# Optimization experiments

Hardware: AMD Instinct MI355X
Metric: run time of the kernel (lower is better)

Reference implementation:

```python
import jax, jax.numpy as jnp
import numpy as np

INF = 1e10
D_KEY = 64

def setup_inputs() -> dict:
    key = jax.random.key(0)
    k1, k2, k3 = jax.random.split(key, 3)
    B, S, D = 4, 4096, D_KEY
    return {
        "query": jax.random.normal(k1, (B, S, D), dtype=jnp.float32),
        "key": jax.random.normal(k2, (B, S, D), dtype=jnp.float32),
        "value": jax.random.normal(k3, (B, S, D), dtype=jnp.float32),
        "mask": jnp.ones((B, S), dtype=jnp.float32),
    }

def reference(query, key, value, mask):
    # dot_products: [B, Sq, Sk]
    dot = jnp.einsum('bqd,bkd->bqk', query, key)
    S = key.shape[1]
    # causal: subtract INF on strict upper triangle (triu(1))
    tri = jnp.triu(jnp.ones((S, S), dtype=dot.dtype), 1) * INF
    dot = dot - tri[None, :, :]
    # additive padding mask: subtract (1-mask)*INF broadcast over query dim
    dot = dot - (1.0 - mask)[:, None, :] * INF
    scale = jnp.sqrt(jnp.float32(D_KEY))
    probs = jax.nn.softmax(dot / scale, axis=-1)  # [B, Sq, Sk]
    # dropout ratio = 0.0 -> identity
    return jnp.einsum('bqk,bkd->bqd', probs, value)
```

## Files before the change

### kernel.cpp

```cpp
#include <hip/hip_runtime.h>
#include <hip/hip_bf16.h>


#define S_LEN  4096
#define N_B    4
#define NT64   64
#define BIGF   1.803368e9f
#define QSCALE (0.125f * 1.44269504089f)
#define FIXMAX 11.0f
#define BIGNEG 1.25e9f
#define MADD_PAD 4224

typedef __attribute__((ext_vector_type(8))) short short8;
typedef __attribute__((ext_vector_type(4))) float f32x4;
typedef __attribute__((ext_vector_type(2))) unsigned int uint2v;
typedef unsigned short ushort_t;

#define KT2_OFF   0
#define KT2_BYTES (N_B * NT64 * 4096 * 2)
#define VT2_OFF   (KT2_OFF + KT2_BYTES)
#define VT2_BYTES (N_B * NT64 * 4096 * 2)
#define NSLOT     (N_B * 184 * 4)
#define OP_OFF    (VT2_OFF + VT2_BYTES)
#define OP_BYTES  (NSLOT * 1024 * 4)
#define PLS_OFF   (OP_OFF + OP_BYTES)
#define PLS_BYTES (NSLOT * 32 * 4)
#define MADD_OFF  (PLS_OFF + PLS_BYTES)
#define MADD_BYTES (N_B * MADD_PAD * 4)
#define WS10_NEEDED (MADD_OFF + MADD_BYTES)

__device__ __forceinline__ unsigned short f2bf(float f) {
    union { float f; unsigned u; } v; v.f = f;
    unsigned r = v.u + 0x7FFF + ((v.u >> 16) & 1);
    return (unsigned short)(r >> 16);
}
__device__ __forceinline__ float bflo(unsigned u) {
    union { unsigned u; float f; } v; v.u = u << 16; return v.f;
}
__device__ __forceinline__ float bfhi(unsigned u) {
    union { unsigned u; float f; } v; v.u = u & 0xffff0000u; return v.f;
}
__device__ __forceinline__ void ld_lds16(const void* g, void* l) {
    __builtin_amdgcn_global_load_lds((const __attribute__((address_space(1))) void*)g,
                                     (__attribute__((address_space(3))) void*)l, 16, 0, 0);
}
__device__ __forceinline__ void ld_lds4(const void* g, void* l) {
    __builtin_amdgcn_global_load_lds((const __attribute__((address_space(1))) void*)g,
                                     (__attribute__((address_space(3))) void*)l, 4, 0, 0);
}


__global__ __launch_bounds__(256)
void prep6(const float* __restrict__ K, const float* __restrict__ V,
           const float* __restrict__ M,
           ushort_t* __restrict__ Kt, ushort_t* __restrict__ Vt,
           float* __restrict__ Madd)
{
    const int t = blockIdx.x, b = blockIdx.y, tid = threadIdx.x;
    ushort_t* ko = Kt + ((size_t)(b * NT64 + t)) * 4096;
    ushort_t* vo = Vt + ((size_t)(b * NT64 + t)) * 4096;
    #pragma unroll
    for (int i = 0; i < 2; ++i) {
        const int idx = tid + 256 * i;
        const int row = idx >> 3, cc = idx & 7;
        const float* src = K + ((size_t)(b * S_LEN + t * 64 + row)) * 64 + cc * 8;
        const f32x4 a = *(const f32x4*)src;
        const f32x4 d4 = *(const f32x4*)(src + 4);
        short8 w;
        w[0]=(short)f2bf(a[0]); w[1]=(short)f2bf(a[1]); w[2]=(short)f2bf(a[2]); w[3]=(short)f2bf(a[3]);
        w[4]=(short)f2bf(d4[0]); w[5]=(short)f2bf(d4[1]); w[6]=(short)f2bf(d4[2]); w[7]=(short)f2bf(d4[3]);
        *(short8*)(ko + row * 64 + ((cc ^ (row & 7)) << 3)) = w;
    }
    #pragma unroll
    for (int i = 0; i < 2; ++i) {
        const int idx = tid + 256 * i;
        const int cc = idx >> 6, d = idx & 63;
        short8 w;
        #pragma unroll
        for (int j = 0; j < 8; ++j)
            w[j] = (short)f2bf(V[((size_t)(b * S_LEN + t * 64 + cc * 8 + j)) * 64 + d]);
        *(short8*)(vo + d * 64 + ((cc ^ (d & 7)) << 3)) = w;
    }
    if (tid < 64) {
        const int k = t * 64 + tid;
        Madd[b * MADD_PAD + k] = (1.0f - M[b * S_LEN + k]) * BIGF;
    }
}

#define PTRANS(PA, PB, PF) do {                                                     \
    unsigned c00_, c01_, c10_, c11_;                                                \
    __asm__("v_cvt_pk_bf16_f32 %0, %1, %2" : "=v"(c00_) : "v"(PA[0]), "v"(PA[1])); \
    __asm__("v_cvt_pk_bf16_f32 %0, %1, %2" : "=v"(c01_) : "v"(PA[2]), "v"(PA[3])); \
    __asm__("v_cvt_pk_bf16_f32 %0, %1, %2" : "=v"(c10_) : "v"(PB[0]), "v"(PB[1])); \
    __asm__("v_cvt_pk_bf16_f32 %0, %1, %2" : "=v"(c11_) : "v"(PB[2]), "v"(PB[3])); \
    uint2v s0_ = __builtin_amdgcn_permlane32_swap(c00_, c10_, false, false);        \
    uint2v s1_ = __builtin_amdgcn_permlane32_swap(c01_, c11_, false, false);        \
    unsigned a0_ = s0_.x, b0_ = s0_.y, a1_ = s1_.x, b1_ = s1_.y;                    \
    __asm__("v_permlane16_swap_b32 %0, %1" : "+v"(a0_), "+v"(b0_));                 \
    __asm__("v_permlane16_swap_b32 %0, %1" : "+v"(a1_), "+v"(b1_));                 \
    union { unsigned u[4]; short8 s; } pw_;                                         \
    pw_.u[0] = a0_;                                                                 \
    pw_.u[1] = a1_;                                                                 \
    pw_.u[2] = b0_;                                                                 \
    pw_.u[3] = b1_;                                                                 \
    PF = pw_.s;                                                                     \
} while (0)

#define CMASK(SV, BB, QG) do {                     \
    _Pragma("unroll")                              \
    for (int r_ = 0; r_ < 4; ++r_)                 \
        if ((BB) + r_ > (QG)) SV[r_] -= BIGF;      \
} while (0)

__global__ __launch_bounds__(256, 3)
void attn_fa13(const float* __restrict__ Q, const ushort_t* __restrict__ Kt,
               const ushort_t* __restrict__ Vt, const float* __restrict__ Madd,
               unsigned* __restrict__ Opu, float* __restrict__ Pll,
               float* __restrict__ O)
{
    const int x = 186 - blockIdx.x;
    const int b = blockIdx.y;
    int v = 1;
    #pragma unroll
    for (int vv = 2; vv <= 11; ++vv) v += (x >= (3 * vv * (vv - 1)) / 2) ? 1 : 0;
    const int y  = x - (3 * v * (v - 1)) / 2;
    const int T  = 3 * (v - 1) + y / v;
    const int c  = y - (y / v) * v;
    const int nt = 2 * T + 2;
    const int t0 = 6 * c;
    const int t1 = (t0 + 6 < nt) ? t0 + 6 : nt;

    const int wid  = threadIdx.x >> 6;
    const int lane = threadIdx.x & 63, l15 = lane & 15, g = lane >> 4;
    const int qbase = T * 128 + wid * 32;
    const int dtile = 2 * T + (wid >> 1);
    const int qg0 = 32 * (wid & 1) + l15 - 4 * g;
    const int qg1 = qg0 + 16;

    __shared__ __attribute__((aligned(16))) ushort_t Kb[3][4096];
    __shared__ __attribute__((aligned(16))) ushort_t Vb[3][4096];
    __shared__ __attribute__((aligned(16))) float    Ml[3][4][64];

    const float* Q0 = Q + ((size_t)(b * S_LEN + qbase + l15)) * 64 + g * 8;
    short8 qA0, qA1, qB0, qB1;
    {
        const f32x4 a0 = *(const f32x4*)(Q0);
        const f32x4 a1 = *(const f32x4*)(Q0 + 4);
        const f32x4 a2 = *(const f32x4*)(Q0 + 32);
        const f32x4 a3 = *(const f32x4*)(Q0 + 36);
        const float* Q1 = Q0 + 16 * 64;
        const f32x4 b0 = *(const f32x4*)(Q1);
        const f32x4 b1 = *(const f32x4*)(Q1 + 4);
        const f32x4 b2 = *(const f32x4*)(Q1 + 32);
        const f32x4 b3 = *(const f32x4*)(Q1 + 36);
        #pragma unroll
        for (int j = 0; j < 4; ++j) {
            qA0[j]     = (short)f2bf(a0[j] * QSCALE);
            qA0[4 + j] = (short)f2bf(a1[j] * QSCALE);
            qA1[j]     = (short)f2bf(a2[j] * QSCALE);
            qA1[4 + j] = (short)f2bf(a3[j] * QSCALE);
            qB0[j]     = (short)f2bf(b0[j] * QSCALE);
            qB0[4 + j] = (short)f2bf(b1[j] * QSCALE);
            qB1[j]     = (short)f2bf(b2[j] * QSCALE);
            qB1[4 + j] = (short)f2bf(b3[j] * QSCALE);
        }
    }
    short8 ones8;
    #pragma unroll
    for (int j = 0; j < 8; ++j) ones8[j] = (short)0x3F80;

    const char*  KtB  = (const char*)Kt + (size_t)b * (NT64 * 8192);
    const char*  VtB  = (const char*)Vt + (size_t)b * (NT64 * 8192);
    const float* MaBs = Madd + (size_t)b * MADD_PAD;

    f32x4 accA[5], accB[5];
    #pragma unroll
    for (int dt = 0; dt < 5; ++dt) {
        accA[dt] = (f32x4){0.f, 0.f, 0.f, 0.f};
        accB[dt] = (f32x4){0.f, 0.f, 0.f, 0.f};
    }

    auto stage = [&](int sl, int t_) {
        const char* kg = KtB + (size_t)t_ * 8192 + wid * 2048 + lane * 16;
        char* kl = (char*)&Kb[sl][0] + wid * 2048;
        ld_lds16(kg,        kl);
        ld_lds16(kg + 1024, kl + 1024);
        const char* vg = VtB + (size_t)t_ * 8192 + wid * 2048 + lane * 16;
        char* vl = (char*)&Vb[sl][0] + wid * 2048;
        ld_lds16(vg,        vl);
        ld_lds16(vg + 1024, vl + 1024);
        ld_lds4 (MaBs + (size_t)t_ * 64 + lane, &Ml[sl][wid][0]);
    };

    stage(0, t0);
    if (t0 + 1 < t1) stage(1, t0 + 1);

    const int ch0 = ((g ^ (l15 & 7)) << 3);
    const int ch1 = (((4 | g) ^ (l15 & 7)) << 3);

    int sc = 0;
    for (int t = t0; t < t1; ++t) {
        if (t + 1 < t1) {
            __asm__ volatile("s_waitcnt vmcnt(5)" ::: "memory");
        } else {
            __asm__ volatile("s_waitcnt vmcnt(0)" ::: "memory");
        }
        __builtin_amdgcn_s_barrier();
        __builtin_amdgcn_sched_barrier(0);

        const int sn = (sc + 2 > 2) ? sc - 1 : sc + 2;
        if (t + 2 < t1) stage(sn, t + 2);

        if (t <= dtile) {
            const ushort_t* kbase = &Kb[sc][0];
            const ushort_t* vbase = &Vb[sc][0];
            const float*    mlw   = &Ml[sc][wid][0];
            const f32x4 z_ = (f32x4){0.f, 0.f, 0.f, 0.f};

            #pragma unroll
            for (int h = 0; h < 2; ++h) {
                const int rb = 32 * h;
                const int chh = h ? ch1 : ch0;
                const f32x4 mmE = *(const f32x4*)(mlw + rb + 4 * g);
                const f32x4 mmO = *(const f32x4*)(mlw + rb + 16 + 4 * g);

                short8 ke0 = *(const short8*)(kbase + ((rb + l15) << 6) + ch0);
                short8 ke1 = *(const short8*)(kbase + ((rb + l15) << 6) + ch1);
                short8 ko0 = *(const short8*)(kbase + ((rb + 16 + l15) << 6) + ch0);
                short8 ko1 = *(const short8*)(kbase + ((rb + 16 + l15) << 6) + ch1);

                f32x4 sEA = __builtin_amdgcn_mfma_f32_16x16x32_bf16(ke0, qA0, z_, 0, 0, 0);
                f32x4 sOA = __builtin_amdgcn_mfma_f32_16x16x32_bf16(ko0, qA0, z_, 0, 0, 0);
                f32x4 sEB = __builtin_amdgcn_mfma_f32_16x16x32_bf16(ke0, qB0, z_, 0, 0, 0);
                f32x4 sOB = __builtin_amdgcn_mfma_f32_16x16x32_bf16(ko0, qB0, z_, 0, 0, 0);
                sEA = __builtin_amdgcn_mfma_f32_16x16x32_bf16(ke1, qA1, sEA, 0, 0, 0);
                sOA = __builtin_amdgcn_mfma_f32_16x16x32_bf16(ko1, qA1, sOA, 0, 0, 0);
                sEB = __builtin_amdgcn_mfma_f32_16x16x32_bf16(ke1, qB1, sEB, 0, 0, 0);
                sOB = __builtin_amdgcn_mfma_f32_16x16x32_bf16(ko1, qB1, sOB, 0, 0, 0);

                sEA -= mmE; sOA -= mmO; sEB -= mmE; sOB -= mmO;
                if (t == dtile) {
                    CMASK(sEA, rb, qg0);      CMASK(sOA, rb + 16, qg0);
                    CMASK(sEB, rb, qg1);      CMASK(sOB, rb + 16, qg1);
                }

                float pEA[4], pOA[4], pEB[4], pOB[4];
                #pragma unroll
                for (int r = 0; r < 4; ++r) {
                    pEA[r] = exp2f(sEA[r] - FIXMAX);
                    pOA[r] = exp2f(sOA[r] - FIXMAX);
                    pEB[r] = exp2f(sEB[r] - FIXMAX);
                    pOB[r] = exp2f(sOB[r] - FIXMAX);
                }

                short8 pfA, pfB;
                PTRANS(pEA, pOA, pfA);
                PTRANS(pEB, pOB, pfB);

                short8 v0 = *(const short8*)(vbase + ((0  + l15) << 6) + chh);
                short8 v1 = *(const short8*)(vbase + ((16 + l15) << 6) + chh);
                short8 v2 = *(const short8*)(vbase + ((32 + l15) << 6) + chh);
                short8 v3 = *(const short8*)(vbase + ((48 + l15) << 6) + chh);
                __builtin_amdgcn_s_setprio(1);
                accA[0] = __builtin_amdgcn_mfma_f32_16x16x32_bf16(pfA, v0, accA[0], 0, 0, 0);
                accA[1] = __builtin_amdgcn_mfma_f32_16x16x32_bf16(pfA, v1, accA[1], 0, 0, 0);
                accA[2] = __builtin_amdgcn_mfma_f32_16x16x32_bf16(pfA, v2, accA[2], 0, 0, 0);
                accA[3] = __builtin_amdgcn_mfma_f32_16x16x32_bf16(pfA, v3, accA[3], 0, 0, 0);
                accA[4] = __builtin_amdgcn_mfma_f32_16x16x32_bf16(pfA, ones8, accA[4], 0, 0, 0);
                accB[0] = __builtin_amdgcn_mfma_f32_16x16x32_bf16(pfB, v0, accB[0], 0, 0, 0);
                accB[1] = __builtin_amdgcn_mfma_f32_16x16x32_bf16(pfB, v1, accB[1], 0, 0, 0);
                accB[2] = __builtin_amdgcn_mfma_f32_16x16x32_bf16(pfB, v2, accB[2], 0, 0, 0);
                accB[3] = __builtin_amdgcn_mfma_f32_16x16x32_bf16(pfB, v3, accB[3], 0, 0, 0);
                accB[4] = __builtin_amdgcn_mfma_f32_16x16x32_bf16(pfB, ones8, accB[4], 0, 0, 0);
                __builtin_amdgcn_s_setprio(0);
            }
        }
        sc = (sc == 2) ? 0 : sc + 1;
    }

    if (v == 1) {
        float* Ob = O + ((size_t)(b * S_LEN + qbase)) * 64;
        #pragma unroll
        for (int r = 0; r < 4; ++r) {
            const float ila = 1.0f / accA[4][r];
            const float ilb = 1.0f / accB[4][r];
            #pragma unroll
            for (int dt = 0; dt < 4; ++dt) {
                Ob[(4 * g + r) * 64 + 16 * dt + l15]      = accA[dt][r] * ila;
                Ob[(16 + 4 * g + r) * 64 + 16 * dt + l15] = accB[dt][r] * ilb;
            }
        }
    } else {
        const int slot = (b * 184 + (x - 3)) * 4 + wid;
        unsigned* Os = Opu + (size_t)slot * 1024;
        #pragma unroll
        for (int dt = 0; dt < 4; ++dt) {
            unsigned u0, u1, u2, u3;
            __asm__("v_cvt_pk_bf16_f32 %0, %1, %2" : "=v"(u0) : "v"(accA[dt][0]), "v"(accA[dt][1]));
            __asm__("v_cvt_pk_bf16_f32 %0, %1, %2" : "=v"(u1) : "v"(accA[dt][2]), "v"(accA[dt][3]));
            __asm__("v_cvt_pk_bf16_f32 %0, %1, %2" : "=v"(u2) : "v"(accB[dt][0]), "v"(accB[dt][1]));
            __asm__("v_cvt_pk_bf16_f32 %0, %1, %2" : "=v"(u3) : "v"(accB[dt][2]), "v"(accB[dt][3]));
            const int d = 16 * dt + l15;
            Os[(2 * g + 0) * 64 + d]     = u0;
            Os[(2 * g + 1) * 64 + d]     = u1;
            Os[(8 + 2 * g + 0) * 64 + d] = u2;
            Os[(8 + 2 * g + 1) * 64 + d] = u3;
        }
        if (l15 == 0) {
            #pragma unroll
            for (int r = 0; r < 4; ++r) {
                Pll[slot * 32 + 4 * g + r]      = accA[4][r];
                Pll[slot * 32 + 16 + 4 * g + r] = accB[4][r];
            }
        }
    }
}

__global__ __launch_bounds__(256)
void combine6(const unsigned* __restrict__ Opu, const float* __restrict__ Pll,
              float* __restrict__ O)
{
    const int bx = blockIdx.x, b = blockIdx.y;
    const int T = 3 + (bx >> 2), wv = bx & 3;
    const int v = (T + 3) / 3;
    const int x0 = (3 * v * (v - 1)) / 2 + (T - 3 * (v - 1)) * v;
    const int sb = (b * 184 + (x0 - 3)) * 4 + wv;
    const int tid = threadIdx.x, rg = tid >> 6, d = tid & 63;

    float a[8] = {0.f,0.f,0.f,0.f,0.f,0.f,0.f,0.f};
    float l[8] = {0.f,0.f,0.f,0.f,0.f,0.f,0.f,0.f};
    for (int cc = 0; cc < v; ++cc) {
        const int sl = sb + 4 * cc;
        const unsigned* base = &Opu[(size_t)sl * 1024 + d];
        const unsigned w0 = base[(4 * rg + 0) * 64];
        const unsigned w1 = base[(4 * rg + 1) * 64];
        const unsigned w2 = base[(4 * rg + 2) * 64];
        const unsigned w3 = base[(4 * rg + 3) * 64];
        a[0] += bflo(w0); a[1] += bfhi(w0);
        a[2] += bflo(w1); a[3] += bfhi(w1);
        a[4] += bflo(w2); a[5] += bfhi(w2);
        a[6] += bflo(w3); a[7] += bfhi(w3);
        #pragma unroll
        for (int j = 0; j < 8; ++j)
            l[j] += Pll[sl * 32 + 8 * rg + j];
    }
    float* Ob = O + ((size_t)(b * S_LEN + T * 128 + wv * 32 + 8 * rg)) * 64 + d;
    #pragma unroll
    for (int j = 0; j < 8; ++j)
        Ob[(size_t)j * 64] = a[j] / l[j];
}


__global__ __launch_bounds__(256)
void attn_fwd_fb(const float* __restrict__ Q, const float* __restrict__ K,
                 const float* __restrict__ V, const float* __restrict__ M,
                 float* __restrict__ O)
{
    const int tile  = blockIdx.x;
    const int b     = blockIdx.y;
    const int qbase = tile * 64;
    const int tid   = threadIdx.x;
    const int wave  = tid >> 6;
    const int lane  = tid & 63;
    const int l15   = lane & 15;
    const int g     = lane >> 4;

    __shared__ __attribute__((aligned(16))) unsigned short Klds[32 * 64];
    __shared__ __attribute__((aligned(16))) unsigned short Vtlds[64 * 40];
    __shared__ __attribute__((aligned(16))) unsigned short Plds[4][16 * 40];

    const float* Qb = Q + ((size_t)b * S_LEN + qbase) * 64;
    const float* Kb = K + (size_t)b * S_LEN * 64;
    const float* Vb = V + (size_t)b * S_LEN * 64;
    const float* Mb = M + (size_t)b * S_LEN;

    const int qrow = 16 * wave + l15;
    short8 qf[2];
    #pragma unroll
    for (int dc = 0; dc < 2; ++dc) {
        const float* src = Qb + (size_t)qrow * 64 + dc * 32 + g * 8;
        #pragma unroll
        for (int j = 0; j < 8; ++j) qf[dc][j] = (short)f2bf(src[j] * 0.125f);
    }

    f32x4 acc[4];
    #pragma unroll
    for (int dt = 0; dt < 4; ++dt) acc[dt] = (f32x4){0.f, 0.f, 0.f, 0.f};
    float mrow[4], lrow[4];
    #pragma unroll
    for (int r = 0; r < 4; ++r) { mrow[r] = -1e30f; lrow[r] = 0.f; }

    const int q_max_wave = qbase + 16 * wave + 15;
    const int nkv = (qbase + 64) / 32;

    for (int it = 0; it < nkv; ++it) {
        const int kv = it * 32;
        __syncthreads();
        {
            const int k = tid >> 3, c = tid & 7;
            const float* src = Kb + (size_t)(kv + k) * 64 + c * 8;
            short8 t8;
            #pragma unroll
            for (int j = 0; j < 8; ++j) t8[j] = (short)f2bf(src[j]);
            const int byte = k * 128 + ((c * 16) ^ ((k & 7) << 4));
            *(short8*)((char*)Klds + byte) = t8;
        }
        {
            const int k = tid & 31, dch = tid >> 5;
            const float* src = Vb + (size_t)(kv + k) * 64 + dch * 8;
            #pragma unroll
            for (int j = 0; j < 8; ++j)
                Vtlds[(dch * 8 + j) * 40 + k] = f2bf(src[j]);
        }
        __syncthreads();

        if (kv > q_max_wave) continue;

        f32x4 s[2];
        s[0] = (f32x4){0.f,0.f,0.f,0.f};
        s[1] = (f32x4){0.f,0.f,0.f,0.f};
        #pragma unroll
        for (int kt = 0; kt < 2; ++kt) {
            const int krow = 16 * kt + l15;
            #pragma unroll
            for (int dc = 0; dc < 2; ++dc) {
                const int byte = krow * 128 + ((dc * 64 + g * 16) ^ ((krow & 7) << 4));
                short8 kf = *(const short8*)((const char*)Klds + byte);
                s[kt] = __builtin_amdgcn_mfma_f32_16x16x32_bf16(qf[dc], kf, s[kt], 0, 0, 0);
            }
        }

        float mk0 = Mb[kv + l15];
        float mk1 = Mb[kv + 16 + l15];
        #pragma unroll
        for (int kt = 0; kt < 2; ++kt) {
            const int gk = kv + 16 * kt + l15;
            const float madd = (1.0f - (kt ? mk1 : mk0)) * BIGNEG;
            #pragma unroll
            for (int r = 0; r < 4; ++r) {
                const int gq = qbase + 16 * wave + 4 * g + r;
                float vv = s[kt][r] - madd;
                if (gk > gq) vv -= BIGNEG;
                s[kt][r] = vv;
            }
        }

        float pexp[2][4], alpha[4];
        #pragma unroll
        for (int r = 0; r < 4; ++r) {
            float tm = fmaxf(s[0][r], s[1][r]);
            #pragma unroll
            for (int off = 8; off >= 1; off >>= 1)
                tm = fmaxf(tm, __shfl_xor(tm, off, 64));
            const float mnew = fmaxf(mrow[r], tm);
            const float a  = __expf(mrow[r] - mnew);
            const float p0 = __expf(s[0][r] - mnew);
            const float p1 = __expf(s[1][r] - mnew);
            float rs = p0 + p1;
            #pragma unroll
            for (int off = 8; off >= 1; off >>= 1)
                rs += __shfl_xor(rs, off, 64);
            lrow[r] = lrow[r] * a + rs;
            mrow[r] = mnew;
            alpha[r] = a;
            pexp[0][r] = p0; pexp[1][r] = p1;
        }

        #pragma unroll
        for (int dt = 0; dt < 4; ++dt)
            #pragma unroll
            for (int r = 0; r < 4; ++r)
                acc[dt][r] *= alpha[r];

        unsigned short* P = Plds[wave];
        #pragma unroll
        for (int kt = 0; kt < 2; ++kt)
            #pragma unroll
            for (int r = 0; r < 4; ++r)
                P[(4 * g + r) * 40 + 16 * kt + l15] = f2bf(pexp[kt][r]);

        __asm__ volatile("s_waitcnt lgkmcnt(0)" ::: "memory");

        short8 pf = *(const short8*)((const char*)P + (l15 * 40 + g * 8) * 2);
        #pragma unroll
        for (int dt = 0; dt < 4; ++dt) {
            short8 vf = *(const short8*)((const char*)Vtlds + ((dt * 16 + l15) * 40 + g * 8) * 2);
            acc[dt] = __builtin_amdgcn_mfma_f32_16x16x32_bf16(pf, vf, acc[dt], 0, 0, 0);
        }
    }

    float* Ob = O + ((size_t)b * S_LEN + qbase) * 64;
    #pragma unroll
    for (int r = 0; r < 4; ++r) {
        const float inv = 1.0f / lrow[r];
        const int row = 16 * wave + 4 * g + r;
        #pragma unroll
        for (int dt = 0; dt < 4; ++dt)
            Ob[(size_t)row * 64 + dt * 16 + l15] = acc[dt][r] * inv;
    }
}

extern "C" void kernel_launch(void* const* d_in, const int* in_sizes, int n_in,
                              void* d_out, int out_size, void* d_ws, size_t ws_size,
                              hipStream_t stream) {
    const float* Q = (const float*)d_in[0];
    const float* K = (const float*)d_in[1];
    const float* V = (const float*)d_in[2];
    const float* M = (const float*)d_in[3];
    float* O = (float*)d_out;

    if (ws_size >= (size_t)WS10_NEEDED) {
        ushort_t* Kt = (ushort_t*)((char*)d_ws + KT2_OFF);
        ushort_t* Vt = (ushort_t*)((char*)d_ws + VT2_OFF);
        unsigned* Op = (unsigned*)((char*)d_ws + OP_OFF);
        float*    Pll= (float*)((char*)d_ws + PLS_OFF);
        float*    Ma = (float*)((char*)d_ws + MADD_OFF);
        prep6<<<dim3(NT64, N_B), 256, 0, stream>>>(K, V, M, Kt, Vt, Ma);
        attn_fa13<<<dim3(187, N_B), 256, 0, stream>>>(Q, Kt, Vt, Ma, Op, Pll, O);
        combine6<<<dim3(116, N_B), 256, 0, stream>>>(Op, Pll, O);
    } else {
        dim3 grid(S_LEN / 64, N_B);
        attn_fwd_fb<<<grid, 256, 0, stream>>>(Q, K, V, M, O);
    }
}
```

Baseline: 40.49 us.

## Fuse prep, attention and combine into one cooperative kernel with grid syncs

Merges the three kernels (K/V bf16 conversion, split attention, partial-result combine) into a single cooperative launch that separates the phases with grid-wide barriers. This removes two kernel launch gaps and the tail/ramp between dependent kernels. The launch first checks occupancy (748 blocks need at least 3 per CU across 256 CUs) and falls back to the three-kernel path otherwise. The cost is two grid.sync barriers, the cooperative launch overhead, and all blocks waiting on the slowest attention block before combine starts.

```diff
diff --git a/kernel.cpp b/kernel.cpp
--- a/kernel.cpp
+++ b/kernel.cpp
@@ -1,5 +1,8 @@
 #include <hip/hip_runtime.h>
 #include <hip/hip_bf16.h>
+#include <hip/hip_cooperative_groups.h>
+
+namespace cg = cooperative_groups;
 
 
 #define S_LEN  4096
@@ -10,6 +13,8 @@
 #define FIXMAX 11.0f
 #define BIGNEG 1.25e9f
 #define MADD_PAD 4224
+#define NJOB   187
+#define NGRID  (NJOB * N_B)
 
 typedef __attribute__((ext_vector_type(8))) short short8;
 typedef __attribute__((ext_vector_type(4))) float f32x4;
@@ -47,44 +52,6 @@
 __device__ __forceinline__ void ld_lds4(const void* g, void* l) {
     __builtin_amdgcn_global_load_lds((const __attribute__((address_space(1))) void*)g,
                                      (__attribute__((address_space(3))) void*)l, 4, 0, 0);
-}
-
-
-__global__ __launch_bounds__(256)
-void prep6(const float* __restrict__ K, const float* __restrict__ V,
-           const float* __restrict__ M,
-           ushort_t* __restrict__ Kt, ushort_t* __restrict__ Vt,
-           float* __restrict__ Madd)
-{
-    const int t = blockIdx.x, b = blockIdx.y, tid = threadIdx.x;
-    ushort_t* ko = Kt + ((size_t)(b * NT64 + t)) * 4096;
-    ushort_t* vo = Vt + ((size_t)(b * NT64 + t)) * 4096;
-    #pragma unroll
-    for (int i = 0; i < 2; ++i) {
-        const int idx = tid + 256 * i;
-        const int row = idx >> 3, cc = idx & 7;
-        const float* src = K + ((size_t)(b * S_LEN + t * 64 + row)) * 64 + cc * 8;
-        const f32x4 a = *(const f32x4*)src;
-        const f32x4 d4 = *(const f32x4*)(src + 4);
-        short8 w;
-        w[0]=(short)f2bf(a[0]); w[1]=(short)f2bf(a[1]); w[2]=(short)f2bf(a[2]); w[3]=(short)f2bf(a[3]);
-        w[4]=(short)f2bf(d4[0]); w[5]=(short)f2bf(d4[1]); w[6]=(short)f2bf(d4[2]); w[7]=(short)f2bf(d4[3]);
-        *(short8*)(ko + row * 64 + ((cc ^ (row & 7)) << 3)) = w;
-    }
-    #pragma unroll
-    for (int i = 0; i < 2; ++i) {
-        const int idx = tid + 256 * i;
-        const int cc = idx >> 6, d = idx & 63;
-        short8 w;
-        #pragma unroll
-        for (int j = 0; j < 8; ++j)
-            w[j] = (short)f2bf(V[((size_t)(b * S_LEN + t * 64 + cc * 8 + j)) * 64 + d]);
-        *(short8*)(vo + d * 64 + ((cc ^ (d & 7)) << 3)) = w;
-    }
-    if (tid < 64) {
-        const int k = t * 64 + tid;
-        Madd[b * MADD_PAD + k] = (1.0f - M[b * S_LEN + k]) * BIGF;
-    }
 }
 
 #define PTRANS(PA, PB, PF) do {                                                     \
@@ -112,14 +79,49 @@
         if ((BB) + r_ > (QG)) SV[r_] -= BIGF;      \
 } while (0)
 
-__global__ __launch_bounds__(256, 3)
-void attn_fa13(const float* __restrict__ Q, const ushort_t* __restrict__ Kt,
-               const ushort_t* __restrict__ Vt, const float* __restrict__ Madd,
-               unsigned* __restrict__ Opu, float* __restrict__ Pll,
-               float* __restrict__ O)
-{
-    const int x = 186 - blockIdx.x;
-    const int b = blockIdx.y;
+
+__device__ __forceinline__ void prep_body(int t, int b, int tid,
+    const float* __restrict__ K, const float* __restrict__ V,
+    const float* __restrict__ M,
+    ushort_t* __restrict__ Kt, ushort_t* __restrict__ Vt,
+    float* __restrict__ Madd)
+{
+    ushort_t* ko = Kt + ((size_t)(b * NT64 + t)) * 4096;
+    ushort_t* vo = Vt + ((size_t)(b * NT64 + t)) * 4096;
+    #pragma unroll
+    for (int i = 0; i < 2; ++i) {
+        const int idx = tid + 256 * i;
+        const int row = idx >> 3, cc = idx & 7;
+        const float* src = K + ((size_t)(b * S_LEN + t * 64 + row)) * 64 + cc * 8;
+        const f32x4 a = *(const f32x4*)src;
+        const f32x4 d4 = *(const f32x4*)(src + 4);
+        short8 w;
+        w[0]=(short)f2bf(a[0]); w[1]=(short)f2bf(a[1]); w[2]=(short)f2bf(a[2]); w[3]=(short)f2bf(a[3]);
+        w[4]=(short)f2bf(d4[0]); w[5]=(short)f2bf(d4[1]); w[6]=(short)f2bf(d4[2]); w[7]=(short)f2bf(d4[3]);
+        *(short8*)(ko + row * 64 + ((cc ^ (row & 7)) << 3)) = w;
+    }
+    #pragma unroll
+    for (int i = 0; i < 2; ++i) {
+        const int idx = tid + 256 * i;
+        const int cc = idx >> 6, d = idx & 63;
+        short8 w;
+        #pragma unroll
+        for (int j = 0; j < 8; ++j)
+            w[j] = (short)f2bf(V[((size_t)(b * S_LEN + t * 64 + cc * 8 + j)) * 64 + d]);
+        *(short8*)(vo + d * 64 + ((cc ^ (d & 7)) << 3)) = w;
+    }
+    if (tid < 64) {
+        const int k = t * 64 + tid;
+        Madd[b * MADD_PAD + k] = (1.0f - M[b * S_LEN + k]) * BIGF;
+    }
+}
+
+__device__ __forceinline__ void attn_body(int x, int b, int tid,
+    ushort_t* Kb , ushort_t* Vb , float* Ml ,
+    const float* __restrict__ Q, const ushort_t* __restrict__ Kt,
+    const ushort_t* __restrict__ Vt, const float* __restrict__ Madd,
+    unsigned* __restrict__ Opu, float* __restrict__ Pll, float* __restrict__ O)
+{
     int v = 1;
     #pragma unroll
     for (int vv = 2; vv <= 11; ++vv) v += (x >= (3 * vv * (vv - 1)) / 2) ? 1 : 0;
@@ -130,16 +132,12 @@
     const int t0 = 6 * c;
     const int t1 = (t0 + 6 < nt) ? t0 + 6 : nt;
 
-    const int wid  = threadIdx.x >> 6;
-    const int lane = threadIdx.x & 63, l15 = lane & 15, g = lane >> 4;
+    const int wid  = tid >> 6;
+    const int lane = tid & 63, l15 = lane & 15, g = lane >> 4;
     const int qbase = T * 128 + wid * 32;
     const int dtile = 2 * T + (wid >> 1);
     const int qg0 = 32 * (wid & 1) + l15 - 4 * g;
     const int qg1 = qg0 + 16;
-
-    __shared__ __attribute__((aligned(16))) ushort_t Kb[3][4096];
-    __shared__ __attribute__((aligned(16))) ushort_t Vb[3][4096];
-    __shared__ __attribute__((aligned(16))) float    Ml[3][4][64];
 
     const float* Q0 = Q + ((size_t)(b * S_LEN + qbase + l15)) * 64 + g * 8;
     short8 qA0, qA1, qB0, qB1;
@@ -182,14 +180,14 @@
 
     auto stage = [&](int sl, int t_) {
         const char* kg = KtB + (size_t)t_ * 8192 + wid * 2048 + lane * 16;
-        char* kl = (char*)&Kb[sl][0] + wid * 2048;
+        char* kl = (char*)(Kb + sl * 4096) + wid * 2048;
         ld_lds16(kg,        kl);
         ld_lds16(kg + 1024, kl + 1024);
         const char* vg = VtB + (size_t)t_ * 8192 + wid * 2048 + lane * 16;
-        char* vl = (char*)&Vb[sl][0] + wid * 2048;
+        char* vl = (char*)(Vb + sl * 4096) + wid * 2048;
         ld_lds16(vg,        vl);
         ld_lds16(vg + 1024, vl + 1024);
-        ld_lds4 (MaBs + (size_t)t_ * 64 + lane, &Ml[sl][wid][0]);
+        ld_lds4 (MaBs + (size_t)t_ * 64 + lane, Ml + (sl * 4 + wid) * 64);
     };
 
     stage(0, t0);
@@ -212,9 +210,9 @@
         if (t + 2 < t1) stage(sn, t + 2);
 
         if (t <= dtile) {
-            const ushort_t* kbase = &Kb[sc][0];
-            const ushort_t* vbase = &Vb[sc][0];
-            const float*    mlw   = &Ml[sc][wid][0];
+            const ushort_t* kbase = Kb + sc * 4096;
+            const ushort_t* vbase = Vb + sc * 4096;
+            const float*    mlw   = Ml + (sc * 4 + wid) * 64;
             const f32x4 z_ = (f32x4){0.f, 0.f, 0.f, 0.f};
 
             #pragma unroll
@@ -316,16 +314,15 @@
     }
 }
 
-__global__ __launch_bounds__(256)
-void combine6(const unsigned* __restrict__ Opu, const float* __restrict__ Pll,
-              float* __restrict__ O)
-{
-    const int bx = blockIdx.x, b = blockIdx.y;
+__device__ __forceinline__ void combine_body(int bx, int b, int tid,
+    const unsigned* __restrict__ Opu, const float* __restrict__ Pll,
+    float* __restrict__ O)
+{
     const int T = 3 + (bx >> 2), wv = bx & 3;
     const int v = (T + 3) / 3;
     const int x0 = (3 * v * (v - 1)) / 2 + (T - 3 * (v - 1)) * v;
     const int sb = (b * 184 + (x0 - 3)) * 4 + wv;
-    const int tid = threadIdx.x, rg = tid >> 6, d = tid & 63;
+    const int rg = tid >> 6, d = tid & 63;
 
     float a[8] = {0.f,0.f,0.f,0.f,0.f,0.f,0.f,0.f};
     float l[8] = {0.f,0.f,0.f,0.f,0.f,0.f,0.f,0.f};
@@ -351,6 +348,70 @@
 }
 
 
+__global__ __launch_bounds__(256, 3)
+void attn_mono(const float* __restrict__ Q, const float* __restrict__ K,
+               const float* __restrict__ V, const float* __restrict__ M,
+               ushort_t* __restrict__ Kt, ushort_t* __restrict__ Vt,
+               float* __restrict__ Madd,
+               unsigned* __restrict__ Opu, float* __restrict__ Pll,
+               float* __restrict__ O)
+{
+    cg::grid_group grid = cg::this_grid();
+    const int gid = blockIdx.x;
+    const int tid = threadIdx.x;
+
+    __shared__ __attribute__((aligned(16))) ushort_t Kb[3 * 4096];
+    __shared__ __attribute__((aligned(16))) ushort_t Vb[3 * 4096];
+    __shared__ __attribute__((aligned(16))) float    Ml[3 * 4 * 64];
+
+    if (gid < 256)
+        prep_body(gid & 63, gid >> 6, tid, K, V, M, Kt, Vt, Madd);
+
+    grid.sync();
+
+    {
+        const int b = gid / NJOB;
+        const int x = 186 - (gid - b * NJOB);
+        attn_body(x, b, tid, Kb, Vb, Ml, Q, Kt, Vt, Madd, Opu, Pll, O);
+    }
+
+    grid.sync();
+
+    if (gid < 464)
+        combine_body(gid % 116, gid / 116, tid, Opu, Pll, O);
+}
+
+
+__global__ __launch_bounds__(256)
+void prep6(const float* __restrict__ K, const float* __restrict__ V,
+           const float* __restrict__ M,
+           ushort_t* __restrict__ Kt, ushort_t* __restrict__ Vt,
+           float* __restrict__ Madd)
+{
+    prep_body(blockIdx.x, blockIdx.y, threadIdx.x, K, V, M, Kt, Vt, Madd);
+}
+
+__global__ __launch_bounds__(256, 3)
+void attn_fa13(const float* __restrict__ Q, const ushort_t* __restrict__ Kt,
+               const ushort_t* __restrict__ Vt, const float* __restrict__ Madd,
+               unsigned* __restrict__ Opu, float* __restrict__ Pll,
+               float* __restrict__ O)
+{
+    __shared__ __attribute__((aligned(16))) ushort_t Kb[3 * 4096];
+    __shared__ __attribute__((aligned(16))) ushort_t Vb[3 * 4096];
+    __shared__ __attribute__((aligned(16))) float    Ml[3 * 4 * 64];
+    attn_body(186 - blockIdx.x, blockIdx.y, threadIdx.x, Kb, Vb, Ml,
+              Q, Kt, Vt, Madd, Opu, Pll, O);
+}
+
+__global__ __launch_bounds__(256)
+void combine6(const unsigned* __restrict__ Opu, const float* __restrict__ Pll,
+              float* __restrict__ O)
+{
+    combine_body(blockIdx.x, blockIdx.y, threadIdx.x, Opu, Pll, O);
+}
+
+
 __global__ __launch_bounds__(256)
 void attn_fwd_fb(const float* __restrict__ Q, const float* __restrict__ K,
                  const float* __restrict__ V, const float* __restrict__ M,
@@ -515,8 +576,21 @@
         unsigned* Op = (unsigned*)((char*)d_ws + OP_OFF);
         float*    Pll= (float*)((char*)d_ws + PLS_OFF);
         float*    Ma = (float*)((char*)d_ws + MADD_OFF);
+
+        int blocksPerCU = 0;
+        hipError_t qerr = hipOccupancyMaxActiveBlocksPerMultiprocessor(
+            &blocksPerCU, (const void*)attn_mono, 256, 0);
+        bool coop_ok = (qerr == hipSuccess) && (blocksPerCU * 256 >= NGRID);
+        if (coop_ok) {
+            void* args[] = { (void*)&Q, (void*)&K, (void*)&V, (void*)&M,
+                             (void*)&Kt, (void*)&Vt, (void*)&Ma,
+                             (void*)&Op, (void*)&Pll, (void*)&O };
+            hipError_t lerr = hipLaunchCooperativeKernel(
+                (const void*)attn_mono, dim3(NGRID), dim3(256), args, 0, stream);
+            if (lerr == hipSuccess) return;
+        }
         prep6<<<dim3(NT64, N_B), 256, 0, stream>>>(K, V, M, Kt, Vt, Ma);
-        attn_fa13<<<dim3(187, N_B), 256, 0, stream>>>(Q, Kt, Vt, Ma, Op, Pll, O);
+        attn_fa13<<<dim3(NJOB, N_B), 256, 0, stream>>>(Q, Kt, Vt, Ma, Op, Pll, O);
         combine6<<<dim3(116, N_B), 256, 0, stream>>>(Op, Pll, O);
     } else {
         dim3 grid(S_LEN / 64, N_B);
```

Measured after the change: 40.63 us. No clear change (+0.3%).

## Fuse split-KV combine into attention kernel via last-block atomic counter

Applied to the files above, without the earlier changes.

Removes the separate combine kernel launch. Each split-KV block publishes its partial output, then increments a per-query-tile atomic counter. The block that arrives last performs the reduction and writes the final output. Counters are zeroed in the prep kernel. This saves one launch and its tail, at the cost of threadfences, an atomic, and a serialized combine on the last-arriving block.

```diff
diff --git a/kernel.cpp b/kernel.cpp
--- a/kernel.cpp
+++ b/kernel.cpp
@@ -10,6 +10,7 @@
 #define FIXMAX 11.0f
 #define BIGNEG 1.25e9f
 #define MADD_PAD 4224
+#define NJOB   187
 
 typedef __attribute__((ext_vector_type(8))) short short8;
 typedef __attribute__((ext_vector_type(4))) float f32x4;
@@ -27,7 +28,9 @@
 #define PLS_BYTES (NSLOT * 32 * 4)
 #define MADD_OFF  (PLS_OFF + PLS_BYTES)
 #define MADD_BYTES (N_B * MADD_PAD * 4)
-#define WS10_NEEDED (MADD_OFF + MADD_BYTES)
+#define CNT_OFF   (MADD_OFF + MADD_BYTES)
+#define CNT_BYTES (N_B * 29 * 4)
+#define WS11_NEEDED (CNT_OFF + CNT_BYTES)
 
 __device__ __forceinline__ unsigned short f2bf(float f) {
     union { float f; unsigned u; } v; v.f = f;
@@ -47,44 +50,6 @@
 __device__ __forceinline__ void ld_lds4(const void* g, void* l) {
     __builtin_amdgcn_global_load_lds((const __attribute__((address_space(1))) void*)g,
                                      (__attribute__((address_space(3))) void*)l, 4, 0, 0);
-}
-
-
-__global__ __launch_bounds__(256)
-void prep6(const float* __restrict__ K, const float* __restrict__ V,
-           const float* __restrict__ M,
-           ushort_t* __restrict__ Kt, ushort_t* __restrict__ Vt,
-           float* __restrict__ Madd)
-{
-    const int t = blockIdx.x, b = blockIdx.y, tid = threadIdx.x;
-    ushort_t* ko = Kt + ((size_t)(b * NT64 + t)) * 4096;
-    ushort_t* vo = Vt + ((size_t)(b * NT64 + t)) * 4096;
-    #pragma unroll
-    for (int i = 0; i < 2; ++i) {
-        const int idx = tid + 256 * i;
-        const int row = idx >> 3, cc = idx & 7;
-        const float* src = K + ((size_t)(b * S_LEN + t * 64 + row)) * 64 + cc * 8;
-        const f32x4 a = *(const f32x4*)src;
-        const f32x4 d4 = *(const f32x4*)(src + 4);
-        short8 w;
-        w[0]=(short)f2bf(a[0]); w[1]=(short)f2bf(a[1]); w[2]=(short)f2bf(a[2]); w[3]=(short)f2bf(a[3]);
-        w[4]=(short)f2bf(d4[0]); w[5]=(short)f2bf(d4[1]); w[6]=(short)f2bf(d4[2]); w[7]=(short)f2bf(d4[3]);
-        *(short8*)(ko + row * 64 + ((cc ^ (row & 7)) << 3)) = w;
-    }
-    #pragma unroll
-    for (int i = 0; i < 2; ++i) {
-        const int idx = tid + 256 * i;
-        const int cc = idx >> 6, d = idx & 63;
-        short8 w;
-        #pragma unroll
-        for (int j = 0; j < 8; ++j)
-            w[j] = (short)f2bf(V[((size_t)(b * S_LEN + t * 64 + cc * 8 + j)) * 64 + d]);
-        *(short8*)(vo + d * 64 + ((cc ^ (d & 7)) << 3)) = w;
-    }
-    if (tid < 64) {
-        const int k = t * 64 + tid;
-        Madd[b * MADD_PAD + k] = (1.0f - M[b * S_LEN + k]) * BIGF;
-    }
 }
 
 #define PTRANS(PA, PB, PF) do {                                                     \
@@ -112,11 +77,83 @@
         if ((BB) + r_ > (QG)) SV[r_] -= BIGF;      \
 } while (0)
 
+
+__global__ __launch_bounds__(256)
+void prep6(const float* __restrict__ K, const float* __restrict__ V,
+           const float* __restrict__ M,
+           ushort_t* __restrict__ Kt, ushort_t* __restrict__ Vt,
+           float* __restrict__ Madd, unsigned* __restrict__ Cnt)
+{
+    const int t = blockIdx.x, b = blockIdx.y, tid = threadIdx.x;
+    ushort_t* ko = Kt + ((size_t)(b * NT64 + t)) * 4096;
+    ushort_t* vo = Vt + ((size_t)(b * NT64 + t)) * 4096;
+    #pragma unroll
+    for (int i = 0; i < 2; ++i) {
+        const int idx = tid + 256 * i;
+        const int row = idx >> 3, cc = idx & 7;
+        const float* src = K + ((size_t)(b * S_LEN + t * 64 + row)) * 64 + cc * 8;
+        const f32x4 a = *(const f32x4*)src;
+        const f32x4 d4 = *(const f32x4*)(src + 4);
+        short8 w;
+        w[0]=(short)f2bf(a[0]); w[1]=(short)f2bf(a[1]); w[2]=(short)f2bf(a[2]); w[3]=(short)f2bf(a[3]);
+        w[4]=(short)f2bf(d4[0]); w[5]=(short)f2bf(d4[1]); w[6]=(short)f2bf(d4[2]); w[7]=(short)f2bf(d4[3]);
+        *(short8*)(ko + row * 64 + ((cc ^ (row & 7)) << 3)) = w;
+    }
+    #pragma unroll
+    for (int i = 0; i < 2; ++i) {
+        const int idx = tid + 256 * i;
+        const int cc = idx >> 6, d = idx & 63;
+        short8 w;
+        #pragma unroll
+        for (int j = 0; j < 8; ++j)
+            w[j] = (short)f2bf(V[((size_t)(b * S_LEN + t * 64 + cc * 8 + j)) * 64 + d]);
+        *(short8*)(vo + d * 64 + ((cc ^ (d & 7)) << 3)) = w;
+    }
+    if (tid < 64) {
+        const int k = t * 64 + tid;
+        Madd[b * MADD_PAD + k] = (1.0f - M[b * S_LEN + k]) * BIGF;
+    }
+    if (tid == 0 && t < 29)
+        Cnt[b * 29 + t] = 0;
+}
+
+__device__ __forceinline__ void combine_body(int T, int wv, int b, int tid,
+    const unsigned* __restrict__ Opu, const float* __restrict__ Pll,
+    float* __restrict__ O)
+{
+    const int v = (T + 3) / 3;
+    const int x0 = (3 * v * (v - 1)) / 2 + (T - 3 * (v - 1)) * v;
+    const int sb = (b * 184 + (x0 - 3)) * 4 + wv;
+    const int rg = tid >> 6, d = tid & 63;
+
+    float a[8] = {0.f,0.f,0.f,0.f,0.f,0.f,0.f,0.f};
+    float l[8] = {0.f,0.f,0.f,0.f,0.f,0.f,0.f,0.f};
+    for (int cc = 0; cc < v; ++cc) {
+        const int sl = sb + 4 * cc;
+        const unsigned* base = &Opu[(size_t)sl * 1024 + d];
+        const unsigned w0 = base[(4 * rg + 0) * 64];
+        const unsigned w1 = base[(4 * rg + 1) * 64];
+        const unsigned w2 = base[(4 * rg + 2) * 64];
+        const unsigned w3 = base[(4 * rg + 3) * 64];
+        a[0] += bflo(w0); a[1] += bfhi(w0);
+        a[2] += bflo(w1); a[3] += bfhi(w1);
+        a[4] += bflo(w2); a[5] += bfhi(w2);
+        a[6] += bflo(w3); a[7] += bfhi(w3);
+        #pragma unroll
+        for (int j = 0; j < 8; ++j)
+            l[j] += Pll[sl * 32 + 8 * rg + j];
+    }
+    float* Ob = O + ((size_t)(b * S_LEN + T * 128 + wv * 32 + 8 * rg)) * 64 + d;
+    #pragma unroll
+    for (int j = 0; j < 8; ++j)
+        Ob[(size_t)j * 64] = a[j] / l[j];
+}
+
 __global__ __launch_bounds__(256, 3)
-void attn_fa13(const float* __restrict__ Q, const ushort_t* __restrict__ Kt,
+void attn_fa14(const float* __restrict__ Q, const ushort_t* __restrict__ Kt,
                const ushort_t* __restrict__ Vt, const float* __restrict__ Madd,
                unsigned* __restrict__ Opu, float* __restrict__ Pll,
-               float* __restrict__ O)
+               unsigned* __restrict__ Cnt, float* __restrict__ O)
 {
     const int x = 186 - blockIdx.x;
     const int b = blockIdx.y;
@@ -140,6 +177,7 @@
     __shared__ __attribute__((aligned(16))) ushort_t Kb[3][4096];
     __shared__ __attribute__((aligned(16))) ushort_t Vb[3][4096];
     __shared__ __attribute__((aligned(16))) float    Ml[3][4][64];
+    __shared__ int lastFlag;
 
     const float* Q0 = Q + ((size_t)(b * S_LEN + qbase + l15)) * 64 + g * 8;
     short8 qA0, qA1, qB0, qB1;
@@ -290,7 +328,10 @@
                 Ob[(16 + 4 * g + r) * 64 + 16 * dt + l15] = accB[dt][r] * ilb;
             }
         }
-    } else {
+        return;
+    }
+
+    {
         const int slot = (b * 184 + (x - 3)) * 4 + wid;
         unsigned* Os = Opu + (size_t)slot * 1024;
         #pragma unroll
@@ -314,40 +355,18 @@
             }
         }
     }
-}
-
-__global__ __launch_bounds__(256)
-void combine6(const unsigned* __restrict__ Opu, const float* __restrict__ Pll,
-              float* __restrict__ O)
-{
-    const int bx = blockIdx.x, b = blockIdx.y;
-    const int T = 3 + (bx >> 2), wv = bx & 3;
-    const int v = (T + 3) / 3;
-    const int x0 = (3 * v * (v - 1)) / 2 + (T - 3 * (v - 1)) * v;
-    const int sb = (b * 184 + (x0 - 3)) * 4 + wv;
-    const int tid = threadIdx.x, rg = tid >> 6, d = tid & 63;
-
-    float a[8] = {0.f,0.f,0.f,0.f,0.f,0.f,0.f,0.f};
-    float l[8] = {0.f,0.f,0.f,0.f,0.f,0.f,0.f,0.f};
-    for (int cc = 0; cc < v; ++cc) {
-        const int sl = sb + 4 * cc;
-        const unsigned* base = &Opu[(size_t)sl * 1024 + d];
-        const unsigned w0 = base[(4 * rg + 0) * 64];
-        const unsigned w1 = base[(4 * rg + 1) * 64];
-        const unsigned w2 = base[(4 * rg + 2) * 64];
-        const unsigned w3 = base[(4 * rg + 3) * 64];
-        a[0] += bflo(w0); a[1] += bfhi(w0);
-        a[2] += bflo(w1); a[3] += bfhi(w1);
-        a[4] += bflo(w2); a[5] += bfhi(w2);
-        a[6] += bflo(w3); a[7] += bfhi(w3);
-        #pragma unroll
-        for (int j = 0; j < 8; ++j)
-            l[j] += Pll[sl * 32 + 8 * rg + j];
-    }
-    float* Ob = O + ((size_t)(b * S_LEN + T * 128 + wv * 32 + 8 * rg)) * 64 + d;
-    #pragma unroll
-    for (int j = 0; j < 8; ++j)
-        Ob[(size_t)j * 64] = a[j] / l[j];
+
+    __threadfence();
+    __syncthreads();
+    if (threadIdx.x == 0)
+        lastFlag = (int)atomicAdd(&Cnt[b * 29 + (T - 3)], 1u);
+    __syncthreads();
+    if (lastFlag == v - 1) {
+        __threadfence();
+        #pragma unroll
+        for (int wv = 0; wv < 4; ++wv)
+            combine_body(T, wv, b, threadIdx.x, Opu, Pll, O);
+    }
 }
 
 
@@ -509,15 +528,15 @@
     const float* M = (const float*)d_in[3];
     float* O = (float*)d_out;
 
-    if (ws_size >= (size_t)WS10_NEEDED) {
+    if (ws_size >= (size_t)WS11_NEEDED) {
         ushort_t* Kt = (ushort_t*)((char*)d_ws + KT2_OFF);
         ushort_t* Vt = (ushort_t*)((char*)d_ws + VT2_OFF);
         unsigned* Op = (unsigned*)((char*)d_ws + OP_OFF);
         float*    Pll= (float*)((char*)d_ws + PLS_OFF);
         float*    Ma = (float*)((char*)d_ws + MADD_OFF);
-        prep6<<<dim3(NT64, N_B), 256, 0, stream>>>(K, V, M, Kt, Vt, Ma);
-        attn_fa13<<<dim3(187, N_B), 256, 0, stream>>>(Q, Kt, Vt, Ma, Op, Pll, O);
-        combine6<<<dim3(116, N_B), 256, 0, stream>>>(Op, Pll, O);
+        unsigned* Cn = (unsigned*)((char*)d_ws + CNT_OFF);
+        prep6<<<dim3(NT64, N_B), 256, 0, stream>>>(K, V, M, Kt, Vt, Ma, Cn);
+        attn_fa14<<<dim3(NJOB, N_B), 256, 0, stream>>>(Q, Kt, Vt, Ma, Op, Pll, Cn, O);
     } else {
         dim3 grid(S_LEN / 64, N_B);
         attn_fwd_fb<<<grid, 256, 0, stream>>>(Q, K, V, M, O);
```

New measurement: 150.2 us. 3.71x slower.
